# Kernel optimization log

Hardware: AMD Instinct MI355X
Metric: run time of the kernel (lower is better)

The kernel has to match this reference:

```python
import jax, jax.numpy as jnp
import numpy as np

LN_EPS = 1e-5


def setup_inputs() -> dict:
    key = jax.random.key(0)
    k1, k2, k3 = jax.random.split(key, 3)
    B, T, D, H = 16, 512, 512, 1024
    x = jax.random.normal(k1, (B, T, D), dtype=jnp.float32)
    # nn.Linear weights: W in R^{2H x D}, U in R^{2H x H} (kaiming-ish scale)
    W_w = jax.random.normal(k2, (2 * H, D), dtype=jnp.float32) * (1.0 / np.sqrt(D))
    U_w = jax.random.normal(k3, (2 * H, H), dtype=jnp.float32) * (1.0 / np.sqrt(H))
    ln_gamma = jnp.ones((2 * H,), dtype=jnp.float32)
    ln_beta = jnp.zeros((2 * H,), dtype=jnp.float32)
    h0 = jnp.zeros((1, H), dtype=jnp.float32)
    return {"x": x, "W_w": W_w, "U_w": U_w, "ln_gamma": ln_gamma,
            "ln_beta": ln_beta, "h0": h0}


def _layernorm(w, gamma, beta):
    mu = jnp.mean(w, axis=-1, keepdims=True)
    var = jnp.mean(jnp.square(w - mu), axis=-1, keepdims=True)
    return (w - mu) * jax.lax.rsqrt(var + LN_EPS) * gamma + beta


def reference(x, W_w, U_w, ln_gamma, ln_beta, h0):
    # Input projection: w = x @ W^T -> [B, T, 2H], then LayerNorm over 2H
    w = jnp.einsum('btd,gd->btg', x, W_w)
    w = _layernorm(w, ln_gamma, ln_beta)

    B = x.shape[0]
    H = U_w.shape[1]
    ht0 = jnp.broadcast_to(h0, (B, H))
    U_t = U_w.T  # [H, 2H]

    def step(ht, wt):  # wt: [B, 2H]
        gates = wt + ht @ U_t
        at, zt = jnp.split(gates, 2, axis=1)
        zt = jax.nn.sigmoid(zt)
        hcand = jax.nn.relu(at)  # drop_mask = 1.0 in eval mode
        ht = zt * ht + (1.0 - zt) * hcand
        return ht, ht

    _, hs = jax.lax.scan(step, ht0, jnp.swapaxes(w, 0, 1))  # hs: [T, B, H]
    return jnp.swapaxes(hs, 0, 1)  # [B, T, H]
```

## Files before the change

### kernel.cpp

```cpp
#include <hip/hip_runtime.h>
#include <hip/hip_cooperative_groups.h>
#include <cmath>

typedef __bf16 bf16x8 __attribute__((ext_vector_type(8)));
typedef float floatx4 __attribute__((ext_vector_type(4)));
typedef unsigned ux4 __attribute__((ext_vector_type(4)));
typedef unsigned short u16;

#define B_ 16
#define T_ 512
#define D_ 512
#define H_ 1024
#define G_ 2048
#define BH (B_ * H_)
#define HP 1032

__global__ void cast_f32_bf16(const float* __restrict__ src, u16* __restrict__ dst, int n) {
  int i = blockIdx.x * blockDim.x + threadIdx.x;
  int stride = gridDim.x * blockDim.x;
  for (; i < n; i += stride) {
    __bf16 b = (__bf16)src[i];
    dst[i] = *reinterpret_cast<u16*>(&b);
  }
}

__launch_bounds__(256, 1)
__global__ void gemm_xW(const u16* __restrict__ xb, const u16* __restrict__ Wb,
                        float* __restrict__ w) {
  const int lane = threadIdx.x & 63;
  const int wv = threadIdx.x >> 6;
  const int rt0 = blockIdx.x * 16;
  const int bidx = rt0 >> 9;
  const int t0 = rt0 & 511;
  const int am = lane & 15;
  const int kq = lane >> 4;

  bf16x8 af[16];
  {
    const u16* xrow = xb + (size_t)(rt0 + am) * D_ + kq * 8;
#pragma unroll
    for (int kk = 0; kk < 16; ++kk)
      af[kk] = *reinterpret_cast<const bf16x8*>(xrow + kk * 32);
  }

#pragma unroll 1
  for (int nt = 0; nt < 32; ++nt) {
    const int n0 = wv * 512 + nt * 16;
    floatx4 acc = {0.f, 0.f, 0.f, 0.f};
    const u16* wrow = Wb + (size_t)(n0 + am) * D_ + kq * 8;
#pragma unroll
    for (int kk = 0; kk < 16; ++kk) {
      bf16x8 bfr = *reinterpret_cast<const bf16x8*>(wrow + kk * 32);
      acc = __builtin_amdgcn_mfma_f32_16x16x32_bf16(af[kk], bfr, acc, 0, 0, 0);
    }
#pragma unroll
    for (int i = 0; i < 4; ++i) {
      int m = kq * 4 + i;
      w[(size_t)((t0 + m) * 16 + bidx) * G_ + n0 + am] = acc[i];
    }
  }
}

__launch_bounds__(256, 1)
__global__ void layernorm_rows(float* __restrict__ w, const float* __restrict__ gamma,
                               const float* __restrict__ beta) {
  float* r = w + (size_t)blockIdx.x * G_;
  float v[8];
  float s = 0.f, ss = 0.f;
#pragma unroll
  for (int i = 0; i < 8; ++i) {
    v[i] = r[threadIdx.x + i * 256];
    s += v[i];
    ss += v[i] * v[i];
  }
#pragma unroll
  for (int d = 1; d < 64; d <<= 1) {
    s += __shfl_xor(s, d, 64);
    ss += __shfl_xor(ss, d, 64);
  }
  __shared__ float ls[4], lss[4];
  const int wv = threadIdx.x >> 6;
  if ((threadIdx.x & 63) == 0) { ls[wv] = s; lss[wv] = ss; }
  __syncthreads();
  float S = ls[0] + ls[1] + ls[2] + ls[3];
  float SS = lss[0] + lss[1] + lss[2] + lss[3];
  float mu = S * (1.f / 2048.f);
  float var = SS * (1.f / 2048.f) - mu * mu;
  float rs = rsqrtf(var + 1e-5f);
#pragma unroll
  for (int i = 0; i < 8; ++i) {
    int g = threadIdx.x + i * 256;
    r[g] = (v[i] - mu) * rs * gamma[g] + beta[g];
  }
}

__launch_bounds__(512, 2)
__global__ void ligru_scan(const float* __restrict__ w, const u16* __restrict__ Ub,
                           const float* __restrict__ h0, float* __restrict__ out,
                           unsigned* __restrict__ hbuf) {
  const int tid = threadIdx.x;
  const int lane = tid & 63;
  const int wv = tid >> 6;
  const int am = lane & 15;
  const int kq = lane >> 4;
  const int blk = blockIdx.x;
  const int j0 = blk * 32;
  const int jt = wv >> 1;
  const int kh = wv & 1;

  __shared__ u16 lds_h[16 * HP];
  __shared__ float lds_r[4][2][16][16];

  const int grow = (am < 8) ? (j0 + 8 * jt + am) : (H_ + j0 + 8 * jt + (am - 8));

  bf16x8 uf[16];
  {
    const u16* urow = Ub + (size_t)grow * H_ + kh * 512 + kq * 8;
#pragma unroll
    for (int kk = 0; kk < 16; ++kk)
      uf[kk] = *reinterpret_cast<const bf16x8*>(urow + kk * 32);
  }

  const int ub = tid >> 5;
  const int jj = tid & 31;
  const int col = j0 + jj;
  float hreg = h0[col];
  float wa = w[(size_t)ub * G_ + col];
  float wz = w[(size_t)ub * G_ + H_ + col];

  const int scol = 4 * (tid & 255);
  const int sb = tid >> 8;

  {
    __bf16 hb = (__bf16)hreg;
    unsigned pk = ((unsigned)*reinterpret_cast<u16*>(&hb) << 16) | 1u;
    unsigned* pp = hbuf + ub * H_ + col;
    asm volatile("global_store_dword %0, %1, off sc0 sc1"
                 :: "v"(pp), "v"(pk) : "memory");
  }

  for (int t = 0; t < T_; ++t) {
    const unsigned* cur = hbuf + (t & 1) * BH;
    unsigned* nxt = hbuf + ((t + 1) & 1) * BH;
    const unsigned tag = (unsigned)(t + 1);

    ux4 chv[8];
    {
      const unsigned* a0 = cur + 0 * 2048 + 4 * tid;
      const unsigned* a1 = cur + 1 * 2048 + 4 * tid;
      const unsigned* a2 = cur + 2 * 2048 + 4 * tid;
      const unsigned* a3 = cur + 3 * 2048 + 4 * tid;
      const unsigned* a4 = cur + 4 * 2048 + 4 * tid;
      const unsigned* a5 = cur + 5 * 2048 + 4 * tid;
      const unsigned* a6 = cur + 6 * 2048 + 4 * tid;
      const unsigned* a7 = cur + 7 * 2048 + 4 * tid;
      unsigned rounds = 0;
      for (;;) {
        asm volatile(
            "global_load_dwordx4 %0, %8, off sc0 sc1\n\t"
            "global_load_dwordx4 %1, %9, off sc0 sc1\n\t"
            "global_load_dwordx4 %2, %10, off sc0 sc1\n\t"
            "global_load_dwordx4 %3, %11, off sc0 sc1\n\t"
            "global_load_dwordx4 %4, %12, off sc0 sc1\n\t"
            "global_load_dwordx4 %5, %13, off sc0 sc1\n\t"
            "global_load_dwordx4 %6, %14, off sc0 sc1\n\t"
            "global_load_dwordx4 %7, %15, off sc0 sc1\n\t"
            "s_waitcnt vmcnt(0)"
            : "=&v"(chv[0]), "=&v"(chv[1]), "=&v"(chv[2]), "=&v"(chv[3]),
              "=&v"(chv[4]), "=&v"(chv[5]), "=&v"(chv[6]), "=&v"(chv[7])
            : "v"(a0), "v"(a1), "v"(a2), "v"(a3), "v"(a4), "v"(a5), "v"(a6), "v"(a7)
            : "memory");
        unsigned bad = 0;
#pragma unroll
        for (int c = 0; c < 8; ++c)
          bad |= ((chv[c].x ^ tag) | (chv[c].y ^ tag) |
                  (chv[c].z ^ tag) | (chv[c].w ^ tag)) & 0xFFFFu;
        if (!bad) break;
        if (++rounds > (1u << 11)) break;
      }
    }

#pragma unroll
    for (int c = 0; c < 8; ++c) {
      int b = 2 * c + sb;
      unsigned lo = (chv[c].x >> 16) | (chv[c].y & 0xFFFF0000u);
      unsigned hi = (chv[c].z >> 16) | (chv[c].w & 0xFFFF0000u);
      uint2 pk; pk.x = lo; pk.y = hi;
      *reinterpret_cast<uint2*>(&lds_h[b * HP + scol]) = pk;
    }
    __syncthreads();

    floatx4 acc0 = {0, 0, 0, 0}, acc1 = {0, 0, 0, 0};
    {
      const u16* hb = &lds_h[am * HP + kh * 512 + kq * 8];
#pragma unroll
      for (int kk = 0; kk < 8; ++kk) {
        bf16x8 x0 = *reinterpret_cast<const bf16x8*>(hb + (kk + 0) * 32);
        bf16x8 x1 = *reinterpret_cast<const bf16x8*>(hb + (kk + 8) * 32);
        acc0 = __builtin_amdgcn_mfma_f32_16x16x32_bf16(x0, uf[kk + 0], acc0, 0, 0, 0);
        acc1 = __builtin_amdgcn_mfma_f32_16x16x32_bf16(x1, uf[kk + 8], acc1, 0, 0, 0);
      }
    }
    floatx4 acc = acc0 + acc1;

    float wan, wzn;
    {
      int tn = (t + 1 < T_) ? (t + 1) : t;
      const float* wt = w + (size_t)(tn * 16 + ub) * G_;
      wan = wt[col];
      wzn = wt[H_ + col];
    }

#pragma unroll
    for (int i = 0; i < 4; ++i)
      lds_r[jt][kh][kq * 4 + i][am] = acc[i];
    __syncthreads();

    float hn;
    {
      const int tl = jj >> 3, c = jj & 7;
      float a = lds_r[tl][0][ub][c] + lds_r[tl][1][ub][c] + wa;
      float z = lds_r[tl][0][ub][8 + c] + lds_r[tl][1][ub][8 + c] + wz;
      float zs = 1.f / (1.f + __expf(-z));
      hn = zs * hreg + (1.f - zs) * fmaxf(a, 0.f);
      hreg = hn;
      __bf16 hb16 = (__bf16)hn;
      unsigned pk = ((unsigned)*reinterpret_cast<u16*>(&hb16) << 16) | (tag + 1u);
      unsigned* pp = nxt + ub * H_ + col;
      asm volatile("global_store_dword %0, %1, off sc0 sc1"
                   :: "v"(pp), "v"(pk) : "memory");
    }

    __builtin_nontemporal_store(hn, &out[((size_t)ub * T_ + t) * H_ + col]);

    wa = wan; wz = wzn;
  }
}

extern "C" void kernel_launch(void* const* d_in, const int* in_sizes, int n_in,
                              void* d_out, int out_size, void* d_ws, size_t ws_size,
                              hipStream_t stream) {
  (void)in_sizes; (void)n_in; (void)out_size; (void)ws_size;
  const float* x = (const float*)d_in[0];
  const float* Ww = (const float*)d_in[1];
  const float* Uw = (const float*)d_in[2];
  const float* gamma = (const float*)d_in[3];
  const float* beta = (const float*)d_in[4];
  const float* h0 = (const float*)d_in[5];
  float* out = (float*)d_out;

  char* p = (char*)d_ws;
  u16* xb = (u16*)p;      p += (size_t)8192 * 512 * 2;
  u16* Wb = (u16*)p;      p += (size_t)2048 * 512 * 2;
  u16* Ub = (u16*)p;      p += (size_t)2048 * 1024 * 2;
  float* w = (float*)p;   p += (size_t)8192 * 2048 * 4;
  unsigned* hbuf = (unsigned*)p; p += (size_t)2 * BH * 4;

  hipMemsetAsync(hbuf, 0, (size_t)2 * BH * 4, stream);
  cast_f32_bf16<<<512, 256, 0, stream>>>(x, xb, 8192 * 512);
  cast_f32_bf16<<<256, 256, 0, stream>>>(Ww, Wb, 2048 * 512);
  cast_f32_bf16<<<256, 256, 0, stream>>>(Uw, Ub, 2048 * 1024);
  gemm_xW<<<512, 256, 0, stream>>>(xb, Wb, w);
  layernorm_rows<<<8192, 256, 0, stream>>>(w, gamma, beta);

  const float* wc = w;
  const u16* Ubc = Ub;
  void* args[5] = { (void*)&wc, (void*)&Ubc, (void*)&h0, (void*)&out, (void*)&hbuf };
  hipLaunchCooperativeKernel((void*)ligru_scan, dim3(32), dim3(512), args, 0, stream);
}
```

Before: 1.897 ms.

## Split recurrent scan into two batch halves with prefetched flag-polled loads

Each timestep of the persistent LiGRU scan now runs as two half-batch groups of 8 rows. Each group has its own MFMA pass and gate update, and the global load for the next half is issued before it is needed, so the polling latency on the shared h buffer overlaps with compute on the other half. The unused LDS rows are zeroed once, and the loads of w are marked nontemporal. Launch bounds drop to one block per SM to allow more registers. The cost is that MFMA and barrier work per step doubles, since each half pads to 16 rows with zeros, and there are more synchronisations per step.

Result: faster. 1.752 ms (-7.7%).

```diff
diff --git a/kernel.cpp b/kernel.cpp
--- a/kernel.cpp
+++ b/kernel.cpp
@@ -94,7 +94,7 @@
   }
 }
 
-__launch_bounds__(512, 2)
+__launch_bounds__(512, 1)
 __global__ void ligru_scan(const float* __restrict__ w, const u16* __restrict__ Ub,
                            const float* __restrict__ h0, float* __restrict__ out,
                            unsigned* __restrict__ hbuf) {
@@ -111,6 +111,8 @@
   __shared__ u16 lds_h[16 * HP];
   __shared__ float lds_r[4][2][16][16];
 
+  for (int i = tid; i < 8 * HP; i += 512) lds_h[8 * HP + i] = 0;
+
   const int grow = (am < 8) ? (j0 + 8 * jt + am) : (H_ + j0 + 8 * jt + (am - 8));
 
   bf16x8 uf[16];
@@ -124,12 +126,11 @@
   const int ub = tid >> 5;
   const int jj = tid & 31;
   const int col = j0 + jj;
-  float hreg = h0[col];
-  float wa = w[(size_t)ub * G_ + col];
-  float wz = w[(size_t)ub * G_ + H_ + col];
-
   const int scol = 4 * (tid & 255);
   const int sb = tid >> 8;
+  float hreg = h0[col];
+  float wa = __builtin_nontemporal_load(&w[(size_t)ub * G_ + col]);
+  float wz = __builtin_nontemporal_load(&w[(size_t)ub * G_ + H_ + col]);
 
   {
     __bf16 hb = (__bf16)hreg;
@@ -139,102 +140,117 @@
                  :: "v"(pp), "v"(pk) : "memory");
   }
 
+  ux4 chv[4];
+#define ISSUE_BUNDLE(base)                                                   \
+  do {                                                                       \
+    const unsigned* b_ = (base) + 4 * tid;                                   \
+    asm volatile("global_load_dwordx4 %0, %4, off sc0 sc1\n\t"               \
+                 "global_load_dwordx4 %1, %5, off sc0 sc1\n\t"               \
+                 "global_load_dwordx4 %2, %6, off sc0 sc1\n\t"               \
+                 "global_load_dwordx4 %3, %7, off sc0 sc1"                   \
+                 : "=&v"(chv[0]), "=&v"(chv[1]), "=&v"(chv[2]), "=&v"(chv[3])\
+                 : "v"(b_), "v"(b_ + 2048), "v"(b_ + 4096), "v"(b_ + 6144)   \
+                 : "memory");                                                \
+  } while (0)
+
+  ISSUE_BUNDLE(hbuf);
+
   for (int t = 0; t < T_; ++t) {
-    const unsigned* cur = hbuf + (t & 1) * BH;
-    unsigned* nxt = hbuf + ((t + 1) & 1) * BH;
     const unsigned tag = (unsigned)(t + 1);
-
-    ux4 chv[8];
-    {
-      const unsigned* a0 = cur + 0 * 2048 + 4 * tid;
-      const unsigned* a1 = cur + 1 * 2048 + 4 * tid;
-      const unsigned* a2 = cur + 2 * 2048 + 4 * tid;
-      const unsigned* a3 = cur + 3 * 2048 + 4 * tid;
-      const unsigned* a4 = cur + 4 * 2048 + 4 * tid;
-      const unsigned* a5 = cur + 5 * 2048 + 4 * tid;
-      const unsigned* a6 = cur + 6 * 2048 + 4 * tid;
-      const unsigned* a7 = cur + 7 * 2048 + 4 * tid;
-      unsigned rounds = 0;
-      for (;;) {
-        asm volatile(
-            "global_load_dwordx4 %0, %8, off sc0 sc1\n\t"
-            "global_load_dwordx4 %1, %9, off sc0 sc1\n\t"
-            "global_load_dwordx4 %2, %10, off sc0 sc1\n\t"
-            "global_load_dwordx4 %3, %11, off sc0 sc1\n\t"
-            "global_load_dwordx4 %4, %12, off sc0 sc1\n\t"
-            "global_load_dwordx4 %5, %13, off sc0 sc1\n\t"
-            "global_load_dwordx4 %6, %14, off sc0 sc1\n\t"
-            "global_load_dwordx4 %7, %15, off sc0 sc1\n\t"
-            "s_waitcnt vmcnt(0)"
-            : "=&v"(chv[0]), "=&v"(chv[1]), "=&v"(chv[2]), "=&v"(chv[3]),
-              "=&v"(chv[4]), "=&v"(chv[5]), "=&v"(chv[6]), "=&v"(chv[7])
-            : "v"(a0), "v"(a1), "v"(a2), "v"(a3), "v"(a4), "v"(a5), "v"(a6), "v"(a7)
-            : "memory");
-        unsigned bad = 0;
-#pragma unroll
-        for (int c = 0; c < 8; ++c)
-          bad |= ((chv[c].x ^ tag) | (chv[c].y ^ tag) |
-                  (chv[c].z ^ tag) | (chv[c].w ^ tag)) & 0xFFFFu;
-        if (!bad) break;
-        if (++rounds > (1u << 11)) break;
+#pragma unroll 1
+    for (int g = 0; g < 2; ++g) {
+      asm volatile("s_waitcnt vmcnt(0)"
+                   : "+v"(chv[0]), "+v"(chv[1]), "+v"(chv[2]), "+v"(chv[3])
+                   :: "memory");
+      __builtin_amdgcn_sched_barrier(0);
+      unsigned bad = 0;
+#pragma unroll
+      for (int c = 0; c < 4; ++c)
+        bad |= ((chv[c].x ^ tag) | (chv[c].y ^ tag) |
+                (chv[c].z ^ tag) | (chv[c].w ^ tag)) & 0xFFFFu;
+      if (bad) {
+        const unsigned* cb = hbuf + (size_t)(t & 1) * BH + g * 8192 + 4 * tid;
+        unsigned rounds = 0;
+        do {
+          asm volatile(
+              "global_load_dwordx4 %0, %4, off sc0 sc1\n\t"
+              "global_load_dwordx4 %1, %5, off sc0 sc1\n\t"
+              "global_load_dwordx4 %2, %6, off sc0 sc1\n\t"
+              "global_load_dwordx4 %3, %7, off sc0 sc1\n\t"
+              "s_waitcnt vmcnt(0)"
+              : "=&v"(chv[0]), "=&v"(chv[1]), "=&v"(chv[2]), "=&v"(chv[3])
+              : "v"(cb), "v"(cb + 2048), "v"(cb + 4096), "v"(cb + 6144)
+              : "memory");
+          bad = 0;
+#pragma unroll
+          for (int c = 0; c < 4; ++c)
+            bad |= ((chv[c].x ^ tag) | (chv[c].y ^ tag) |
+                    (chv[c].z ^ tag) | (chv[c].w ^ tag)) & 0xFFFFu;
+        } while (bad && ++rounds < 2048u);
+      }
+
+#pragma unroll
+      for (int c = 0; c < 4; ++c) {
+        int b = 2 * c + sb;
+        unsigned lo = (chv[c].x >> 16) | (chv[c].y & 0xFFFF0000u);
+        unsigned hi = (chv[c].z >> 16) | (chv[c].w & 0xFFFF0000u);
+        uint2 pk; pk.x = lo; pk.y = hi;
+        *reinterpret_cast<uint2*>(&lds_h[b * HP + scol]) = pk;
+      }
+      asm volatile("s_waitcnt lgkmcnt(0)" ::: "memory");
+      __builtin_amdgcn_s_barrier();
+      __builtin_amdgcn_sched_barrier(0);
+
+      floatx4 acc0 = {0, 0, 0, 0}, acc1 = {0, 0, 0, 0};
+      {
+        const u16* hb = &lds_h[am * HP + kh * 512 + kq * 8];
+#pragma unroll
+        for (int kk = 0; kk < 8; ++kk) {
+          bf16x8 x0 = *reinterpret_cast<const bf16x8*>(hb + (kk + 0) * 32);
+          bf16x8 x1 = *reinterpret_cast<const bf16x8*>(hb + (kk + 8) * 32);
+          acc0 = __builtin_amdgcn_mfma_f32_16x16x32_bf16(x0, uf[kk + 0], acc0, 0, 0, 0);
+          acc1 = __builtin_amdgcn_mfma_f32_16x16x32_bf16(x1, uf[kk + 8], acc1, 0, 0, 0);
+        }
+      }
+      floatx4 acc = acc0 + acc1;
+
+#pragma unroll
+      for (int i = 0; i < 4; ++i)
+        lds_r[jt][kh][kq * 4 + i][am] = acc[i];
+      asm volatile("s_waitcnt lgkmcnt(0)" ::: "memory");
+      __builtin_amdgcn_s_barrier();
+      __builtin_amdgcn_sched_barrier(0);
+
+      float wan = wa, wzn = wz;
+      if (sb == g) {
+        const int tl = jj >> 3, cc = jj & 7;
+        const int mr = ub & 7;
+        float a = lds_r[tl][0][mr][cc] + lds_r[tl][1][mr][cc] + wa;
+        float z = lds_r[tl][0][mr][8 + cc] + lds_r[tl][1][mr][8 + cc] + wz;
+        float zs = 1.f / (1.f + __expf(-z));
+        float hn = zs * hreg + (1.f - zs) * fmaxf(a, 0.f);
+        hreg = hn;
+        __bf16 hb16 = (__bf16)hn;
+        unsigned pk = ((unsigned)*reinterpret_cast<u16*>(&hb16) << 16) | (tag + 1u);
+        unsigned* pp = hbuf + (size_t)((t + 1) & 1) * BH + ub * H_ + col;
+        asm volatile("global_store_dword %0, %1, off sc0 sc1"
+                     :: "v"(pp), "v"(pk) : "memory");
+        __builtin_nontemporal_store(hn, &out[((size_t)ub * T_ + t) * H_ + col]);
+        int tn = (t + 1 < T_) ? (t + 1) : t;
+        const float* wt = w + (size_t)(tn * 16 + ub) * G_;
+        wan = __builtin_nontemporal_load(&wt[col]);
+        wzn = __builtin_nontemporal_load(&wt[H_ + col]);
+      }
+      wa = wan; wz = wzn;
+
+      {
+        int ntx = (g == 1) ? (t + 1) : t;
+        const unsigned* nb = hbuf + (size_t)(ntx & 1) * BH + (g ^ 1) * 8192;
+        ISSUE_BUNDLE(nb);
       }
     }
-
-#pragma unroll
-    for (int c = 0; c < 8; ++c) {
-      int b = 2 * c + sb;
-      unsigned lo = (chv[c].x >> 16) | (chv[c].y & 0xFFFF0000u);
-      unsigned hi = (chv[c].z >> 16) | (chv[c].w & 0xFFFF0000u);
-      uint2 pk; pk.x = lo; pk.y = hi;
-      *reinterpret_cast<uint2*>(&lds_h[b * HP + scol]) = pk;
-    }
-    __syncthreads();
-
-    floatx4 acc0 = {0, 0, 0, 0}, acc1 = {0, 0, 0, 0};
-    {
-      const u16* hb = &lds_h[am * HP + kh * 512 + kq * 8];
-#pragma unroll
-      for (int kk = 0; kk < 8; ++kk) {
-        bf16x8 x0 = *reinterpret_cast<const bf16x8*>(hb + (kk + 0) * 32);
-        bf16x8 x1 = *reinterpret_cast<const bf16x8*>(hb + (kk + 8) * 32);
-        acc0 = __builtin_amdgcn_mfma_f32_16x16x32_bf16(x0, uf[kk + 0], acc0, 0, 0, 0);
-        acc1 = __builtin_amdgcn_mfma_f32_16x16x32_bf16(x1, uf[kk + 8], acc1, 0, 0, 0);
-      }
-    }
-    floatx4 acc = acc0 + acc1;
-
-    float wan, wzn;
-    {
-      int tn = (t + 1 < T_) ? (t + 1) : t;
-      const float* wt = w + (size_t)(tn * 16 + ub) * G_;
-      wan = wt[col];
-      wzn = wt[H_ + col];
-    }
-
-#pragma unroll
-    for (int i = 0; i < 4; ++i)
-      lds_r[jt][kh][kq * 4 + i][am] = acc[i];
-    __syncthreads();
-
-    float hn;
-    {
-      const int tl = jj >> 3, c = jj & 7;
-      float a = lds_r[tl][0][ub][c] + lds_r[tl][1][ub][c] + wa;
-      float z = lds_r[tl][0][ub][8 + c] + lds_r[tl][1][ub][8 + c] + wz;
-      float zs = 1.f / (1.f + __expf(-z));
-      hn = zs * hreg + (1.f - zs) * fmaxf(a, 0.f);
-      hreg = hn;
-      __bf16 hb16 = (__bf16)hn;
-      unsigned pk = ((unsigned)*reinterpret_cast<u16*>(&hb16) << 16) | (tag + 1u);
-      unsigned* pp = nxt + ub * H_ + col;
-      asm volatile("global_store_dword %0, %1, off sc0 sc1"
-                   :: "v"(pp), "v"(pk) : "memory");
-    }
-
-    __builtin_nontemporal_store(hn, &out[((size_t)ub * T_ + t) * H_ + col]);
-
-    wa = wan; wz = wzn;
-  }
+  }
+#undef ISSUE_BUNDLE
 }
 
 extern "C" void kernel_launch(void* const* d_in, const int* in_sizes, int n_in,
```

## Elect one XCC for recurrent scan and pipeline h loads with loader waves

Applied to the files above, without the earlier changes.

Launches 256 blocks and uses an atomic election on the hardware XCC id, so that exactly 32 blocks on a single XCC do the recurrence while the rest exit. The aim is to keep the cross-block h exchange inside one XCC's L2, which makes flag polling cheaper. It also splits the batch into two halves processed in alternating phases. Loader waves prefetch the next half's h and w from global memory while compute waves run MFMA and the gate update, with the first load using the cheaper sc0 scope. The risks are relying on at least 32 blocks landing on one XCC, added spin overhead, and correctness depending on the memory-scope choices.

Result: faster. 1.775 ms (-6.4%).

```diff
diff --git a/kernel.cpp b/kernel.cpp
--- a/kernel.cpp
+++ b/kernel.cpp
@@ -94,22 +94,38 @@
   }
 }
 
-__launch_bounds__(512, 2)
+__launch_bounds__(512, 1)
 __global__ void ligru_scan(const float* __restrict__ w, const u16* __restrict__ Ub,
                            const float* __restrict__ h0, float* __restrict__ out,
-                           unsigned* __restrict__ hbuf) {
+                           unsigned* __restrict__ hbuf, unsigned* __restrict__ elect) {
+  __shared__ unsigned s_role;
+  if (threadIdx.x == 0) {
+    unsigned xcc;
+    asm volatile("s_getreg_b32 %0, hwreg(HW_REG_XCC_ID)" : "=s"(xcc));
+    xcc &= 7u;
+    unsigned ticket = atomicAdd(&elect[xcc], 1u);
+    if (ticket == 31u) atomicCAS(&elect[8], 0u, xcc + 1u);
+    unsigned wn;
+    while ((wn = atomicAdd(&elect[8], 0u)) == 0u) __builtin_amdgcn_s_sleep(8);
+    s_role = (wn == xcc + 1u && ticket < 32u) ? ticket : 0xFFFFFFFFu;
+  }
+  __syncthreads();
+  const unsigned role = s_role;
+  if (role == 0xFFFFFFFFu) return;
+
   const int tid = threadIdx.x;
   const int lane = tid & 63;
   const int wv = tid >> 6;
   const int am = lane & 15;
   const int kq = lane >> 4;
-  const int blk = blockIdx.x;
-  const int j0 = blk * 32;
-  const int jt = wv >> 1;
-  const int kh = wv & 1;
+  const int j0 = (int)role * 32;
+  const bool loader = (tid >= 256);
+  const int jt = wv & 3;
+  const int kh = wv >> 2;
 
   __shared__ u16 lds_h[16 * HP];
   __shared__ float lds_r[4][2][16][16];
+  __shared__ float lds_w[2][8][2][32];
 
   const int grow = (am < 8) ? (j0 + 8 * jt + am) : (H_ + j0 + 8 * jt + (am - 8));
 
@@ -121,120 +137,164 @@
       uf[kk] = *reinterpret_cast<const bf16x8*>(urow + kk * 32);
   }
 
-  const int ub = tid >> 5;
+  const int bl = tid >> 5;
   const int jj = tid & 31;
   const int col = j0 + jj;
-  float hreg = h0[col];
-  float wa = w[(size_t)ub * G_ + col];
-  float wz = w[(size_t)ub * G_ + H_ + col];
-
-  const int scol = 4 * (tid & 255);
-  const int sb = tid >> 8;
-
-  {
-    __bf16 hb = (__bf16)hreg;
+  float hreg0 = 0.f, hreg1 = 0.f;
+
+  const int li = tid & 255;
+  const int wb = li >> 5;
+  const int wgt = (li >> 4) & 1;
+  const int wc2 = (li & 15) * 2;
+  ux4 chv0, chv1, chv2, chv3, chv4, chv5, chv6, chv7;
+  uint2 wnx;
+
+#define LOADB(SCSTR, cb)                                                          \
+  asm volatile("global_load_dwordx4 %0, %8, off " SCSTR "\n\t"                    \
+               "global_load_dwordx4 %1, %9, off " SCSTR "\n\t"                    \
+               "global_load_dwordx4 %2, %10, off " SCSTR "\n\t"                   \
+               "global_load_dwordx4 %3, %11, off " SCSTR "\n\t"                   \
+               "global_load_dwordx4 %4, %12, off " SCSTR "\n\t"                   \
+               "global_load_dwordx4 %5, %13, off " SCSTR "\n\t"                   \
+               "global_load_dwordx4 %6, %14, off " SCSTR "\n\t"                   \
+               "global_load_dwordx4 %7, %15, off " SCSTR                          \
+               : "=&v"(chv0), "=&v"(chv1), "=&v"(chv2), "=&v"(chv3),              \
+                 "=&v"(chv4), "=&v"(chv5), "=&v"(chv6), "=&v"(chv7)               \
+               : "v"(cb), "v"((cb) + 1024), "v"((cb) + 2048), "v"((cb) + 3072),   \
+                 "v"((cb) + 4096), "v"((cb) + 5120), "v"((cb) + 6144),            \
+                 "v"((cb) + 7168)                                                 \
+               : "memory")
+
+#define TAGCHK(tg)                                                                \
+  ((((chv0.x ^ (tg)) | (chv0.y ^ (tg)) | (chv0.z ^ (tg)) | (chv0.w ^ (tg)) |      \
+     (chv1.x ^ (tg)) | (chv1.y ^ (tg)) | (chv1.z ^ (tg)) | (chv1.w ^ (tg)) |      \
+     (chv2.x ^ (tg)) | (chv2.y ^ (tg)) | (chv2.z ^ (tg)) | (chv2.w ^ (tg)) |      \
+     (chv3.x ^ (tg)) | (chv3.y ^ (tg)) | (chv3.z ^ (tg)) | (chv3.w ^ (tg)) |      \
+     (chv4.x ^ (tg)) | (chv4.y ^ (tg)) | (chv4.z ^ (tg)) | (chv4.w ^ (tg)) |      \
+     (chv5.x ^ (tg)) | (chv5.y ^ (tg)) | (chv5.z ^ (tg)) | (chv5.w ^ (tg)) |      \
+     (chv6.x ^ (tg)) | (chv6.y ^ (tg)) | (chv6.z ^ (tg)) | (chv6.w ^ (tg)) |      \
+     (chv7.x ^ (tg)) | (chv7.y ^ (tg)) | (chv7.z ^ (tg)) | (chv7.w ^ (tg))) &     \
+    0xFFFFu))
+
+#define UNPACK_ROW(C, GG)                                                         \
+  {                                                                               \
+    unsigned lo = (chv##C.x >> 16) | (chv##C.y & 0xFFFF0000u);                    \
+    unsigned hi = (chv##C.z >> 16) | (chv##C.w & 0xFFFF0000u);                    \
+    uint2 pk2; pk2.x = lo; pk2.y = hi;                                            \
+    *reinterpret_cast<uint2*>(&lds_h[((GG) * 8 + (C)) * HP + 4 * li]) = pk2;      \
+  }
+
+  if (!loader) {
+    hreg0 = h0[col];
+    hreg1 = hreg0;
+    __bf16 hb = (__bf16)hreg0;
     unsigned pk = ((unsigned)*reinterpret_cast<u16*>(&hb) << 16) | 1u;
-    unsigned* pp = hbuf + ub * H_ + col;
-    asm volatile("global_store_dword %0, %1, off sc0 sc1"
-                 :: "v"(pp), "v"(pk) : "memory");
-  }
-
+    unsigned* p0 = hbuf + (0 * 8 + bl) * H_ + col;
+    unsigned* p1 = hbuf + (8 + bl) * H_ + col;
+    asm volatile("global_store_dword %0, %2, off sc0 sc1\n\t"
+                 "global_store_dword %1, %2, off sc0 sc1"
+                 :: "v"(p0), "v"(p1), "v"(pk) : "memory");
+  } else {
+    const float* ws = w + (size_t)wb * G_ + wgt * H_ + j0 + wc2;
+    asm volatile("global_load_dwordx2 %0, %1, off nt"
+                 : "=&v"(wnx) : "v"(ws) : "memory");
+    const unsigned* nb = hbuf + 4 * li;
+    LOADB("sc0", nb);
+  }
+
+#define PHASE(GG, HREG)                                                           \
+  {                                                                               \
+    const unsigned tag = (unsigned)(t + 1);                                       \
+    const int tn = (GG == 0) ? t : ((t + 1 < T_) ? (t + 1) : t);                  \
+    const int gn = GG ^ 1;                                                        \
+    if (loader) {                                                                 \
+      asm volatile("s_waitcnt vmcnt(0)"                                           \
+                   : "+v"(chv0), "+v"(chv1), "+v"(chv2), "+v"(chv3),              \
+                     "+v"(chv4), "+v"(chv5), "+v"(chv6), "+v"(chv7),              \
+                     "+v"(wnx) :: "memory");                                      \
+      __builtin_amdgcn_sched_barrier(0);                                          \
+      unsigned bad = TAGCHK(tag);                                                 \
+      if (bad) {                                                                  \
+        const unsigned* cb = hbuf + (size_t)(t & 1) * BH + (GG) * 8192 + 4 * li;  \
+        unsigned rounds = 0;                                                      \
+        do {                                                                      \
+          if (rounds == 0) {                                                      \
+            LOADB("sc0", cb);                                                     \
+          } else {                                                                \
+            __builtin_amdgcn_fence(__ATOMIC_ACQUIRE, "agent");                    \
+            LOADB("sc0 sc1", cb);                                                 \
+          }                                                                       \
+          asm volatile("s_waitcnt vmcnt(0)"                                       \
+                       : "+v"(chv0), "+v"(chv1), "+v"(chv2), "+v"(chv3),          \
+                         "+v"(chv4), "+v"(chv5), "+v"(chv6), "+v"(chv7)           \
+                       :: "memory");                                              \
+          bad = TAGCHK(tag);                                                      \
+        } while (bad && ++rounds < 4096u);                                        \
+      }                                                                           \
+      UNPACK_ROW(0, GG) UNPACK_ROW(1, GG) UNPACK_ROW(2, GG) UNPACK_ROW(3, GG)     \
+      UNPACK_ROW(4, GG) UNPACK_ROW(5, GG) UNPACK_ROW(6, GG) UNPACK_ROW(7, GG)     \
+      *reinterpret_cast<uint2*>(&lds_w[GG][wb][wgt][wc2]) = wnx;                  \
+      asm volatile("s_waitcnt lgkmcnt(0)" ::: "memory");                          \
+                 \
+      {                                                                           \
+        const float* ws = w + (size_t)(tn * 16 + gn * 8 + wb) * G_ +              \
+                          wgt * H_ + j0 + wc2;                                    \
+        asm volatile("global_load_dwordx2 %0, %1, off nt"                         \
+                     : "=&v"(wnx) : "v"(ws) : "memory");                          \
+      }                                                                           \
+    }                                                                             \
+    __builtin_amdgcn_s_barrier();                       \
+    __builtin_amdgcn_sched_barrier(0);                                            \
+    floatx4 acc0 = {0, 0, 0, 0}, acc1 = {0, 0, 0, 0};                             \
+    {                                                                             \
+      const u16* hb = &lds_h[am * HP + kh * 512 + kq * 8];                        \
+      _Pragma("unroll")                                                           \
+      for (int kk = 0; kk < 8; ++kk) {                                            \
+        bf16x8 x0 = *reinterpret_cast<const bf16x8*>(hb + (kk + 0) * 32);         \
+        bf16x8 x1 = *reinterpret_cast<const bf16x8*>(hb + (kk + 8) * 32);         \
+        acc0 = __builtin_amdgcn_mfma_f32_16x16x32_bf16(x0, uf[kk + 0], acc0, 0, 0, 0); \
+        acc1 = __builtin_amdgcn_mfma_f32_16x16x32_bf16(x1, uf[kk + 8], acc1, 0, 0, 0); \
+      }                                                                           \
+    }                                                                             \
+    floatx4 acc = acc0 + acc1;                                                    \
+    _Pragma("unroll")                                                             \
+    for (int i = 0; i < 4; ++i)                                                   \
+      lds_r[jt][kh][kq * 4 + i][am] = acc[i];                                     \
+    asm volatile("s_waitcnt lgkmcnt(0)" ::: "memory");                            \
+    __builtin_amdgcn_s_barrier();                      \
+    __builtin_amdgcn_sched_barrier(0);                                            \
+    if (loader) {                                                                 \
+              \
+      const unsigned* nb = hbuf + (size_t)(tn & 1) * BH + gn * 8192 + 4 * li;     \
+      LOADB("sc0", nb);                                                           \
+    } else {                                                                      \
+      const int tl = jj >> 3, cc = jj & 7;                                        \
+      const int mr = (GG) * 8 + bl;                                               \
+      float a = lds_r[tl][0][mr][cc] + lds_r[tl][1][mr][cc] +                     \
+                lds_w[GG][bl][0][jj];                                             \
+      float z = lds_r[tl][0][mr][8 + cc] + lds_r[tl][1][mr][8 + cc] +             \
+                lds_w[GG][bl][1][jj];                                             \
+      float zs = 1.f / (1.f + __expf(-z));                                        \
+      float hn = zs * (HREG) + (1.f - zs) * fmaxf(a, 0.f);                        \
+      (HREG) = hn;                                                                \
+      __bf16 hb16 = (__bf16)hn;                                                   \
+      unsigned pk = ((unsigned)*reinterpret_cast<u16*>(&hb16) << 16) | (tag + 1u);\
+      unsigned* pp = hbuf + (size_t)((t + 1) & 1) * BH + ((GG) * 8 + bl) * H_ + col; \
+      asm volatile("global_store_dword %0, %1, off sc0 sc1"                       \
+                   :: "v"(pp), "v"(pk) : "memory");                               \
+      __builtin_nontemporal_store(hn, &out[((size_t)((GG) * 8 + bl) * T_ + t) * H_ + col]); \
+    }                                                                             \
+  }
+
+#pragma unroll 1
   for (int t = 0; t < T_; ++t) {
-    const unsigned* cur = hbuf + (t & 1) * BH;
-    unsigned* nxt = hbuf + ((t + 1) & 1) * BH;
-    const unsigned tag = (unsigned)(t + 1);
-
-    ux4 chv[8];
-    {
-      const unsigned* a0 = cur + 0 * 2048 + 4 * tid;
-      const unsigned* a1 = cur + 1 * 2048 + 4 * tid;
-      const unsigned* a2 = cur + 2 * 2048 + 4 * tid;
-      const unsigned* a3 = cur + 3 * 2048 + 4 * tid;
-      const unsigned* a4 = cur + 4 * 2048 + 4 * tid;
-      const unsigned* a5 = cur + 5 * 2048 + 4 * tid;
-      const unsigned* a6 = cur + 6 * 2048 + 4 * tid;
-      const unsigned* a7 = cur + 7 * 2048 + 4 * tid;
-      unsigned rounds = 0;
-      for (;;) {
-        asm volatile(
-            "global_load_dwordx4 %0, %8, off sc0 sc1\n\t"
-            "global_load_dwordx4 %1, %9, off sc0 sc1\n\t"
-            "global_load_dwordx4 %2, %10, off sc0 sc1\n\t"
-            "global_load_dwordx4 %3, %11, off sc0 sc1\n\t"
-            "global_load_dwordx4 %4, %12, off sc0 sc1\n\t"
-            "global_load_dwordx4 %5, %13, off sc0 sc1\n\t"
-            "global_load_dwordx4 %6, %14, off sc0 sc1\n\t"
-            "global_load_dwordx4 %7, %15, off sc0 sc1\n\t"
-            "s_waitcnt vmcnt(0)"
-            : "=&v"(chv[0]), "=&v"(chv[1]), "=&v"(chv[2]), "=&v"(chv[3]),
-              "=&v"(chv[4]), "=&v"(chv[5]), "=&v"(chv[6]), "=&v"(chv[7])
-            : "v"(a0), "v"(a1), "v"(a2), "v"(a3), "v"(a4), "v"(a5), "v"(a6), "v"(a7)
-            : "memory");
-        unsigned bad = 0;
-#pragma unroll
-        for (int c = 0; c < 8; ++c)
-          bad |= ((chv[c].x ^ tag) | (chv[c].y ^ tag) |
-                  (chv[c].z ^ tag) | (chv[c].w ^ tag)) & 0xFFFFu;
-        if (!bad) break;
-        if (++rounds > (1u << 11)) break;
-      }
-    }
-
-#pragma unroll
-    for (int c = 0; c < 8; ++c) {
-      int b = 2 * c + sb;
-      unsigned lo = (chv[c].x >> 16) | (chv[c].y & 0xFFFF0000u);
-      unsigned hi = (chv[c].z >> 16) | (chv[c].w & 0xFFFF0000u);
-      uint2 pk; pk.x = lo; pk.y = hi;
-      *reinterpret_cast<uint2*>(&lds_h[b * HP + scol]) = pk;
-    }
-    __syncthreads();
-
-    floatx4 acc0 = {0, 0, 0, 0}, acc1 = {0, 0, 0, 0};
-    {
-      const u16* hb = &lds_h[am * HP + kh * 512 + kq * 8];
-#pragma unroll
-      for (int kk = 0; kk < 8; ++kk) {
-        bf16x8 x0 = *reinterpret_cast<const bf16x8*>(hb + (kk + 0) * 32);
-        bf16x8 x1 = *reinterpret_cast<const bf16x8*>(hb + (kk + 8) * 32);
-        acc0 = __builtin_amdgcn_mfma_f32_16x16x32_bf16(x0, uf[kk + 0], acc0, 0, 0, 0);
-        acc1 = __builtin_amdgcn_mfma_f32_16x16x32_bf16(x1, uf[kk + 8], acc1, 0, 0, 0);
-      }
-    }
-    floatx4 acc = acc0 + acc1;
-
-    float wan, wzn;
-    {
-      int tn = (t + 1 < T_) ? (t + 1) : t;
-      const float* wt = w + (size_t)(tn * 16 + ub) * G_;
-      wan = wt[col];
-      wzn = wt[H_ + col];
-    }
-
-#pragma unroll
-    for (int i = 0; i < 4; ++i)
-      lds_r[jt][kh][kq * 4 + i][am] = acc[i];
-    __syncthreads();
-
-    float hn;
-    {
-      const int tl = jj >> 3, c = jj & 7;
-      float a = lds_r[tl][0][ub][c] + lds_r[tl][1][ub][c] + wa;
-      float z = lds_r[tl][0][ub][8 + c] + lds_r[tl][1][ub][8 + c] + wz;
-      float zs = 1.f / (1.f + __expf(-z));
-      hn = zs * hreg + (1.f - zs) * fmaxf(a, 0.f);
-      hreg = hn;
-      __bf16 hb16 = (__bf16)hn;
-      unsigned pk = ((unsigned)*reinterpret_cast<u16*>(&hb16) << 16) | (tag + 1u);
-      unsigned* pp = nxt + ub * H_ + col;
-      asm volatile("global_store_dword %0, %1, off sc0 sc1"
-                   :: "v"(pp), "v"(pk) : "memory");
-    }
-
-    __builtin_nontemporal_store(hn, &out[((size_t)ub * T_ + t) * H_ + col]);
-
-    wa = wan; wz = wzn;
-  }
+    PHASE(0, hreg0)
+    PHASE(1, hreg1)
+  }
+#undef PHASE
+#undef LOADB
+#undef TAGCHK
+#undef UNPACK_ROW
 }
 
 extern "C" void kernel_launch(void* const* d_in, const int* in_sizes, int n_in,
@@ -255,8 +315,9 @@
   u16* Ub = (u16*)p;      p += (size_t)2048 * 1024 * 2;
   float* w = (float*)p;   p += (size_t)8192 * 2048 * 4;
   unsigned* hbuf = (unsigned*)p; p += (size_t)2 * BH * 4;
-
-  hipMemsetAsync(hbuf, 0, (size_t)2 * BH * 4, stream);
+  unsigned* elect = (unsigned*)p; p += 64;
+
+  hipMemsetAsync(hbuf, 0, (size_t)2 * BH * 4 + 64, stream);
   cast_f32_bf16<<<512, 256, 0, stream>>>(x, xb, 8192 * 512);
   cast_f32_bf16<<<256, 256, 0, stream>>>(Ww, Wb, 2048 * 512);
   cast_f32_bf16<<<256, 256, 0, stream>>>(Uw, Ub, 2048 * 1024);
@@ -265,6 +326,7 @@
 
   const float* wc = w;
   const u16* Ubc = Ub;
-  void* args[5] = { (void*)&wc, (void*)&Ubc, (void*)&h0, (void*)&out, (void*)&hbuf };
-  hipLaunchCooperativeKernel((void*)ligru_scan, dim3(32), dim3(512), args, 0, stream);
-}
+  void* args[6] = { (void*)&wc, (void*)&Ubc, (void*)&h0, (void*)&out,
+                    (void*)&hbuf, (void*)&elect };
+  hipLaunchCooperativeKernel((void*)ligru_scan, dim3(256), dim3(512), args, 0, stream);
+}
```
